# Optimization experiments

Measured on AMD Instinct MI355X. Metric: run time of the kernel, lower is better.

Reference implementation:

```python
import jax, jax.numpy as jnp
import numpy as np

BS, HS, NH = 8, 3, 8          # block_size, halo_size, num_heads
WIN = BS + 2 * HS             # 14
DQK = 16                      # dim_head_qk = make_divisible(128*1.0)//8
DV = 16                       # dim_head_v = 128 // 8
SCALE = DQK ** -0.5


def _rel_pos_index():
    # Faithful numpy port of QueryFreePosEmbedRel._get_relative_position_index
    w = WIN
    coords = np.stack(np.meshgrid(np.arange(w), np.arange(w), indexing='ij'))  # (2,w,w)
    flat = coords.reshape(2, -1)                                               # (2, w*w)
    rel = flat[:, :, None] - flat[:, None, :]                                  # (2, ww, ww)
    rel = rel.transpose(1, 2, 0).astype(np.int64)
    rel[:, :, 0] += w - 1
    rel[:, :, 1] += w - 1
    rel[:, :, 0] *= 2 * w - 1
    rel = rel.sum(-1).reshape(w, w, w, w)
    sh = (w - BS) // 2  # == halo_size
    rel = rel[sh:sh + BS, sh:sh + BS, :, :].reshape(BS * BS, w * w)
    return rel

_REL_IDX = _rel_pos_index()


def setup_inputs() -> dict:
    key = jax.random.key(0)
    k1, k2, k3, k4, k5, k6 = jax.random.split(key, 6)
    C = 128
    dim_out_qk = NH * DQK   # 128
    dim_out_v = NH * DV     # 128
    x = jax.random.normal(k1, (4, 128, 128, C), dtype=jnp.float32)
    q_w = jax.random.normal(k2, (dim_out_qk, C), dtype=jnp.float32) * 0.05
    kv_w = jax.random.normal(k3, (dim_out_qk + dim_out_v, C), dtype=jnp.float32) * 0.05
    pos_table = jax.random.normal(k4, ((2 * WIN - 1) * (2 * WIN - 1), NH), dtype=jnp.float32) * 0.02
    proj_w = jax.random.normal(k5, (dim_out_v, dim_out_v), dtype=jnp.float32) * 0.05
    proj_b = jax.random.normal(k6, (dim_out_v,), dtype=jnp.float32) * 0.01
    return {"x": x, "q_w": q_w, "kv_w": kv_w, "pos_table": pos_table,
            "proj_w": proj_w, "proj_b": proj_b}


def reference(x, q_w, kv_w, pos_table, proj_w, proj_b):
    B, H, W, C = x.shape  # H,W divisible by BS -> no padding branch
    nhb, nwb = H // BS, W // BS
    nb = nhb * nwb

    # --- queries: (B,NH,nb,bs^2,DQK), block-partitioned ---
    q = x @ q_w.T
    q = q.reshape(B, nhb, BS, nwb, BS, NH, DQK).transpose(0, 5, 1, 3, 2, 4, 6)
    q = q.reshape(B, NH, nb, BS * BS, DQK)

    # --- kv 1x1 conv + halo padding + overlapping window extraction ---
    kv = x @ kv_w.T                                   # (B,H,W, NH*(DQK+DV))
    kv = jnp.pad(kv, ((0, 0), (HS, HS), (HS, HS), (0, 0)))
    ri = (np.arange(nhb) * BS)[:, None] + np.arange(WIN)[None, :]
    ci = (np.arange(nwb) * BS)[:, None] + np.arange(WIN)[None, :]
    kvw = kv[:, ri]
    kvw = kvw[:, :, :, ci]
    kvw = kvw.transpose(0, 1, 3, 2, 4, 5).reshape(B, nb, WIN * WIN, NH, DQK + DV)
    kvw = kvw.transpose(0, 3, 1, 2, 4)
    k = kvw[..., :DQK]
    v = kvw[..., DQK:]

    bias = pos_table[_REL_IDX.reshape(-1)].reshape(BS * BS, WIN * WIN, NH)
    bias = bias.transpose(2, 0, 1)[None, :, None]

    # --- scores + halo-boundary mask + softmax ---
    attn = jnp.einsum('bhnqd,bhnkd->bhnqk', q * SCALE, k) + bias
    ones = jnp.pad(jnp.ones((H, W), jnp.float32), ((HS, HS), (HS, HS)))
    mw = ones[ri][:, :, ci].transpose(0, 2, 1, 3).reshape(nb, WIN * WIN)
    valid = (mw > 0)[None, None, :, None, :]
    attn = jnp.where(valid, attn, -jnp.finfo(attn.dtype).max)
    attn = jax.nn.softmax(attn, axis=-1)

    # --- weighted sum over V, fold blocks back to (B,H,W,dim_out_v) ---
    out = jnp.einsum('bhnqk,bhnkd->bhnqd', attn, v)   # (B,NH,nb,bs^2,DV)
    out = out.reshape(B, NH, nhb, nwb, BS, BS, DV)
    out = out.transpose(0, 2, 4, 3, 5, 1, 6).reshape(B, H, W, NH * DV)
    return out @ proj_w.T + proj_b
```

## Files before the change

kernel.cpp:

```cpp
#include <hip/hip_runtime.h>
#include <float.h>


typedef float f32x4 __attribute__((ext_vector_type(4)));
typedef short s16x4 __attribute__((ext_vector_type(4)));
typedef short s16x8 __attribute__((ext_vector_type(8)));
typedef unsigned int u32x2 __attribute__((ext_vector_type(2)));
typedef unsigned int u32x4 __attribute__((ext_vector_type(4)));

__device__ inline ushort f2bf(float f) {
    unsigned u = __float_as_uint(f);
    return (ushort)((u + 0x7FFF + ((u >> 16) & 1)) >> 16);
}
__device__ inline float bf2f(ushort h) { return __uint_as_float((unsigned)h << 16); }
__device__ inline unsigned cvtpk(float a, float b) {
    unsigned r;
    asm("v_cvt_pk_bf16_f32 %0, %1, %2" : "=v"(r) : "v"(a), "v"(b));
    return r;
}
#if __has_builtin(__builtin_amdgcn_exp2f)
#define EXP2(x) __builtin_amdgcn_exp2f(x)
#else
#define EXP2(x) exp2f(x)
#endif

__global__ __launch_bounds__(256) void conv_w(
    const float* __restrict__ q_w, const float* __restrict__ kv_w,
    const float* __restrict__ proj_w, ushort* whi, ushort* wlo)
{
    const int g = blockIdx.x * 256 + threadIdx.x;
    const int row = g >> 7, col = g & 127;
    const float v = (row < 128) ? q_w[row * 128 + col]
                  : (row < 384) ? kv_w[(row - 128) * 128 + col]
                                : proj_w[(row - 384) * 128 + col];
    const ushort h = f2bf(v);
    const int off = ((row >> 4) * 2048) + ((col >> 3) * 128) + ((row & 15) * 8) + (col & 7);
    whi[off] = h;
    wlo[off] = f2bf(v - bf2f(h));
}

__global__ __launch_bounds__(256) void gemm_split(
    const float* A,
    const ushort* __restrict__ Whi, const ushort* __restrict__ Wlo,
    int wbase, int ntc, int tok1,
    ushort* qb, ushort* kvb, float* outf, const float* __restrict__ bias)
{
    __shared__ ushort Ah[128 * 128];
    __shared__ ushort Al[128 * 128];

    const int t = threadIdx.x;
    const int row0 = blockIdx.x * 128;
    const int w = t >> 6, l = t & 63;
    const int wm = w >> 1, wn = w & 1;
    const int lr = l & 15, cA = l >> 4;

#pragma unroll
    for (int i = 0; i < 16; ++i) {
        const int idx = t + i * 256;
        const int p = idx >> 5, fc = idx & 31;
        const float4 v = *(const float4*)(A + (size_t)(row0 + p) * 128 + fc * 4);
        const int base = p * 128 + (((fc >> 1) ^ (p & 7)) << 3) + (fc & 1) * 4;
        const unsigned h01 = cvtpk(v.x, v.y), h23 = cvtpk(v.z, v.w);
        *(u32x2*)&Ah[base] = (u32x2){h01, h23};
        const float hx = __uint_as_float(h01 << 16);
        const float hy = __uint_as_float(h01 & 0xFFFF0000u);
        const float hz = __uint_as_float(h23 << 16);
        const float hw = __uint_as_float(h23 & 0xFFFF0000u);
        *(u32x2*)&Al[base] = (u32x2){ cvtpk(v.x - hx, v.y - hy),
                                      cvtpk(v.z - hz, v.w - hw) };
    }
    __syncthreads();

#pragma unroll 1
    for (int nt = 0; nt < ntc; ++nt) {
        f32x4 acc[4][4];
#pragma unroll
        for (int mf = 0; mf < 4; ++mf)
#pragma unroll
            for (int nf = 0; nf < 4; ++nf) acc[mf][nf] = (f32x4){0.f,0.f,0.f,0.f};

#pragma unroll 1
        for (int kk = 0; kk < 4; ++kk) {
            s16x8 wh[4], wl[4];
#pragma unroll
            for (int nf = 0; nf < 4; ++nf) {
                const int rb = (wbase >> 4) + nt * 8 + wn * 4 + nf;
                const size_t off = (size_t)rb * 2048 + (kk * 4 + cA) * 128 + lr * 8;
                wh[nf] = *(const s16x8*)&Whi[off];
                wl[nf] = *(const s16x8*)&Wlo[off];
            }
#pragma unroll
            for (int mf = 0; mf < 4; ++mf) {
                const int p = wm * 64 + mf * 16 + lr;
                const int off = p * 128 + ((((kk << 2) + cA) ^ (p & 7)) << 3);
                const s16x8 xh = *(const s16x8*)&Ah[off];
                const s16x8 xl = *(const s16x8*)&Al[off];
#pragma unroll
                for (int nf = 0; nf < 4; ++nf) {
                    acc[mf][nf] = __builtin_amdgcn_mfma_f32_16x16x32_bf16(
                                      wh[nf], xh, acc[mf][nf], 0, 0, 0);
                    acc[mf][nf] = __builtin_amdgcn_mfma_f32_16x16x32_bf16(
                                      wh[nf], xl, acc[mf][nf], 0, 0, 0);
                    acc[mf][nf] = __builtin_amdgcn_mfma_f32_16x16x32_bf16(
                                      wl[nf], xh, acc[mf][nf], 0, 0, 0);
                }
            }
        }

#pragma unroll
        for (int mf = 0; mf < 4; ++mf) {
            const size_t pix = row0 + wm * 64 + mf * 16 + lr;
#pragma unroll
            for (int nf = 0; nf < 4; ++nf) {
                const int chan = wn * 64 + nf * 16 + cA * 4;
                const f32x4 o = acc[mf][nf];
                if (tok1) {
                    const u32x2 pk = (u32x2){ cvtpk(o[0], o[1]), cvtpk(o[2], o[3]) };
                    if (nt == 0) {
                        const int head = wn * 4 + nf;
                        *(u32x2*)(qb + ((size_t)head << 20) + pix * 16 + (chan & 15)) = pk;
                    } else {
                        const int gchan = (nt - 1) * 128 + chan;
                        const int head = gchan >> 5;
                        *(u32x2*)(kvb + ((size_t)head << 21) + pix * 32 + (gchan & 31)) = pk;
                    }
                } else {
                    const float4 bv = *(const float4*)(bias + chan);
                    f32x4 r = o;
                    r[0] += bv.x; r[1] += bv.y; r[2] += bv.z; r[3] += bv.w;
                    *(f32x4*)(outf + pix * 128 + chan) = r;
                }
            }
        }
    }
}

__global__ __launch_bounds__(256) void halo_attn(
    float* out,
    const ushort* __restrict__ qg,
    const ushort* __restrict__ kvg,
    const float* __restrict__ pos_table)
{
    __shared__ ushort VT[2][16][232];
    __shared__ float  bias_l[444];
    __shared__ int    keyoff[256];
    __shared__ ushort vbf[232];

    const int t  = threadIdx.x;
    const int bi = blockIdx.x, head = blockIdx.y, bpair = blockIdx.z;
    const int by = bi >> 4, bx = bi & 15;
    const int w  = t >> 6;
    const int lb = w >> 1;
    const int qh = w & 1;
    const int batch = bpair * 2 + lb;
    const int l  = t & 63;
    const int lr = l & 15;
    const int cA = l >> 4;

    const char* kvh = (const char*)(kvg + ((size_t)head << 21) + ((size_t)batch << 19));

    if (t < 224) {
        const int wy = t >> 4, wx = t & 15;
        const int py = by * 8 + wy - 3, px = bx * 8 + wx - 3;
        const bool valid = (wx < 14) && ((unsigned)py < 128u) && ((unsigned)px < 128u);
        keyoff[t] = valid ? ((py * 128 + px) * 64) : 0;
        vbf[t]    = valid ? (ushort)0x3F80 : (ushort)0;
    } else {
        keyoff[t] = 0;
        if (t < 232) vbf[t] = 0;
    }
    for (int i = t; i < 444; i += 256) {
        float v = 0.f;
        if (i >= 2) {
            const int r = i - 2, ry = r / 21, rx = r - ry * 21;
            v = pos_table[((ry + 3) * 27 + rx + 3) * 8 + head] * 1.44269504f;
        }
        bias_l[i] = v;
    }
    __syncthreads();

#pragma unroll
    for (int it = 0; it < 2; ++it) {
        const int idx = t + it * 256;
        if (idx < 448) {
            const int slb = (idx < 224) ? 0 : 1;
            const int key = idx - slb * 224;
            const char* sb = (const char*)(kvg + ((size_t)head << 21)
                             + ((size_t)(bpair * 2 + slb) << 19));
            const char* src = sb + keyoff[key] + 32;
            const bool valid = vbf[key] != 0;
            const s16x8 z = (s16x8){0,0,0,0,0,0,0,0};
            const s16x8 v0 = valid ? *(const s16x8*)src : z;
            const s16x8 v1 = valid ? *(const s16x8*)(src + 16) : z;
#pragma unroll
            for (int j = 0; j < 8; ++j) {
                VT[slb][j][key]     = (ushort)v0[j];
                VT[slb][j + 8][key] = (ushort)v1[j];
            }
        }
    }
    __syncthreads();

    const int gbase = ((lr >> 2) << 3) + (lr & 3);
    const int wy0 = cA >> 1, wx0 = (cA & 1) * 8;
    const ushort* qhp = qg + ((size_t)head << 20);
    s16x8 qf[2];
    float* optr[2];
    const float* bptr[2];
#pragma unroll
    for (int j = 0; j < 2; ++j) {
        const int q = (qh * 2 + j) * 16 + lr;
        const int qy = q >> 3, qx = q & 7;
        const size_t pix = ((size_t)(batch * 128 + by * 8 + qy)) * 128 + bx * 8 + qx;
        optr[j] = out + pix * 128 + head * 16 + cA * 4;
        bptr[j] = bias_l + 2 + (qy + 13 - wy0) * 21 + (qx + 6 - wx0);
#pragma unroll
        for (int k = 0; k < 8; ++k) qf[j][k] = 0;
        if (cA < 2)
            qf[j] = *(const s16x8*)(qhp + pix * 16 + cA * 8);
    }

    f32x4 accv[2], accs[2];
#pragma unroll
    for (int j = 0; j < 2; ++j) {
        accv[j] = (f32x4){0.f, 0.f, 0.f, 0.f};
        accs[j] = (f32x4){0.f, 0.f, 0.f, 0.f};
    }

    s16x8 ak0 = *(const s16x8*)(kvh + keyoff[gbase]     + cA * 16);
    s16x8 ak1 = *(const s16x8*)(kvh + keyoff[gbase + 4] + cA * 16);

#pragma unroll 1
    for (int m = 0; m < 7; ++m) {
        const int nx = 32 * (m + 1) + gbase;
        const s16x8 nk0 = *(const s16x8*)(kvh + keyoff[nx]     + cA * 16);
        const s16x8 nk1 = *(const s16x8*)(kvh + keyoff[nx + 4] + cA * 16);

        const int kb = 32 * m + cA * 8;
        const s16x8 vt  = *(const s16x8*)&VT[lb][lr][kb];
        const s16x8 vld = *(const s16x8*)&vbf[kb];

#pragma unroll
        for (int j = 0; j < 2; ++j) {
            const f32x4 sf0 = __builtin_amdgcn_mfma_f32_16x16x32_bf16(
                                  ak0, qf[j], (f32x4){0.f, 0.f, 0.f, 0.f}, 0, 0, 0);
            const f32x4 sf1 = __builtin_amdgcn_mfma_f32_16x16x32_bf16(
                                  ak1, qf[j], (f32x4){0.f, 0.f, 0.f, 0.f}, 0, 0, 0);
            const float* bq = bptr[j] - m * 42;
            float pr0[4], pr1[4];
#pragma unroll
            for (int r = 0; r < 4; ++r)
                pr0[r] = EXP2(fmaf(sf0[r], 0.36067376f, bq[7 - r]));
#pragma unroll
            for (int r = 0; r < 4; ++r)
                pr1[r] = EXP2(fmaf(sf1[r], 0.36067376f, bq[3 - r]));

            const u32x4 pk = (u32x4){ cvtpk(pr0[0], pr0[1]), cvtpk(pr0[2], pr0[3]),
                                      cvtpk(pr1[0], pr1[1]), cvtpk(pr1[2], pr1[3]) };
            const s16x8 pb = *(const s16x8*)&pk;
            accv[j] = __builtin_amdgcn_mfma_f32_16x16x32_bf16(vt,  pb, accv[j], 0, 0, 0);
            accs[j] = __builtin_amdgcn_mfma_f32_16x16x32_bf16(vld, pb, accs[j], 0, 0, 0);
        }
        ak0 = nk0;
        ak1 = nk1;
    }

#pragma unroll
    for (int j = 0; j < 2; ++j) {
        const float inv = 1.0f / accs[j][0];
        *(f32x4*)optr[j] = accv[j] * inv;
    }
}

extern "C" void kernel_launch(void* const* d_in, const int* in_sizes, int n_in,
                              void* d_out, int out_size, void* d_ws, size_t ws_size,
                              hipStream_t stream) {
    const float* x      = (const float*)d_in[0];
    const float* q_w    = (const float*)d_in[1];
    const float* kv_w   = (const float*)d_in[2];
    const float* pt     = (const float*)d_in[3];
    const float* proj_w = (const float*)d_in[4];
    const float* proj_b = (const float*)d_in[5];
    float* out = (float*)d_out;

    ushort* ykvb = (ushort*)d_ws;
    ushort* qb   = (ushort*)((char*)d_ws + 33554432);
    ushort* whi  = (ushort*)((char*)d_ws + 33554432 + 16777216);
    ushort* wlo  = whi + 65536;

    const dim3 blk(256);
    conv_w<<<dim3(256), blk, 0, stream>>>(q_w, kv_w, proj_w, whi, wlo);
    gemm_split<<<dim3(512), blk, 0, stream>>>(x, whi, wlo, 0, 3, 1,
                                              qb, ykvb, nullptr, nullptr);
    halo_attn<<<dim3(256, 8, 2), blk, 0, stream>>>(out, qb, ykvb, pt);
    gemm_split<<<dim3(512), blk, 0, stream>>>(out, whi, wlo, 384, 1, 0,
                                              nullptr, nullptr, out, proj_b);
}
```

Before: 90.61 us.

## Process all four batches per halo_attn block and precompute bias table

The halo_attn kernel now uses 512-thread blocks that cover all four batch images for one spatial block and head, instead of two batches per block over a grid z of 2. The keyoff/vbf index setup and the bias table are therefore built once per block for more work. The exp2-scaled relative-position bias table is moved into the weight-conversion kernel, which writes it to workspace, and halo_attn only copies it into shared memory. In exchange there are half as many blocks, each with larger shared memory (VT doubles) and twice the threads, which may lower occupancy or scheduling flexibility.

```diff
diff --git a/kernel.cpp b/kernel.cpp
--- a/kernel.cpp
+++ b/kernel.cpp
@@ -26,17 +26,32 @@
 
 __global__ __launch_bounds__(256) void conv_w(
     const float* __restrict__ q_w, const float* __restrict__ kv_w,
-    const float* __restrict__ proj_w, ushort* whi, ushort* wlo)
+    const float* __restrict__ proj_w, const float* __restrict__ pos_table,
+    ushort* whi, ushort* wlo, float* bias_g)
 {
-    const int g = blockIdx.x * 256 + threadIdx.x;
-    const int row = g >> 7, col = g & 127;
-    const float v = (row < 128) ? q_w[row * 128 + col]
-                  : (row < 384) ? kv_w[(row - 128) * 128 + col]
-                                : proj_w[(row - 384) * 128 + col];
-    const ushort h = f2bf(v);
-    const int off = ((row >> 4) * 2048) + ((col >> 3) * 128) + ((row & 15) * 8) + (col & 7);
-    whi[off] = h;
-    wlo[off] = f2bf(v - bf2f(h));
+    if (blockIdx.x < 256) {
+        const int g = blockIdx.x * 256 + threadIdx.x;
+        const int row = g >> 7, col = g & 127;
+        const float v = (row < 128) ? q_w[row * 128 + col]
+                      : (row < 384) ? kv_w[(row - 128) * 128 + col]
+                                    : proj_w[(row - 384) * 128 + col];
+        const ushort h = f2bf(v);
+        const int off = ((row >> 4) * 2048) + ((col >> 3) * 128)
+                      + ((row & 15) * 8) + (col & 7);
+        whi[off] = h;
+        wlo[off] = f2bf(v - bf2f(h));
+    } else {
+        const int i = (blockIdx.x - 256) * 256 + threadIdx.x;
+        if (i < 8 * 448) {
+            const int h = i / 448, e = i - h * 448;
+            float v = 0.f;
+            if (e >= 2) {
+                const int r = e - 2, ry = r / 21, rx = r - ry * 21;
+                v = pos_table[((ry + 3) * 27 + rx + 3) * 8 + h] * 1.44269504f;
+            }
+            bias_g[h * 448 + e] = v;
+        }
+    }
 }
 
 __global__ __launch_bounds__(256) void gemm_split(
@@ -135,29 +150,28 @@
     }
 }
 
-__global__ __launch_bounds__(256) void halo_attn(
+__global__ __launch_bounds__(512) void halo_attn(
     float* out,
     const ushort* __restrict__ qg,
     const ushort* __restrict__ kvg,
-    const float* __restrict__ pos_table)
+    const float* __restrict__ bias_g)
 {
-    __shared__ ushort VT[2][16][232];
-    __shared__ float  bias_l[444];
+    __shared__ ushort VT[4][16][232];
+    __shared__ float  bias_l[448];
     __shared__ int    keyoff[256];
     __shared__ ushort vbf[232];
 
     const int t  = threadIdx.x;
-    const int bi = blockIdx.x, head = blockIdx.y, bpair = blockIdx.z;
+    const int bi = blockIdx.x, head = blockIdx.y;
     const int by = bi >> 4, bx = bi & 15;
     const int w  = t >> 6;
     const int lb = w >> 1;
     const int qh = w & 1;
-    const int batch = bpair * 2 + lb;
     const int l  = t & 63;
     const int lr = l & 15;
     const int cA = l >> 4;
 
-    const char* kvh = (const char*)(kvg + ((size_t)head << 21) + ((size_t)batch << 19));
+    const char* kvh = (const char*)(kvg + ((size_t)head << 21) + ((size_t)lb << 19));
 
     if (t < 224) {
         const int wy = t >> 4, wx = t & 15;
@@ -165,28 +179,21 @@
         const bool valid = (wx < 14) && ((unsigned)py < 128u) && ((unsigned)px < 128u);
         keyoff[t] = valid ? ((py * 128 + px) * 64) : 0;
         vbf[t]    = valid ? (ushort)0x3F80 : (ushort)0;
-    } else {
+    } else if (t < 256) {
         keyoff[t] = 0;
         if (t < 232) vbf[t] = 0;
     }
-    for (int i = t; i < 444; i += 256) {
-        float v = 0.f;
-        if (i >= 2) {
-            const int r = i - 2, ry = r / 21, rx = r - ry * 21;
-            v = pos_table[((ry + 3) * 27 + rx + 3) * 8 + head] * 1.44269504f;
-        }
-        bias_l[i] = v;
-    }
+    for (int i = t; i < 448; i += 512)
+        bias_l[i] = bias_g[head * 448 + i];
     __syncthreads();
 
 #pragma unroll
-    for (int it = 0; it < 2; ++it) {
-        const int idx = t + it * 256;
-        if (idx < 448) {
-            const int slb = (idx < 224) ? 0 : 1;
-            const int key = idx - slb * 224;
+    for (int rd = 0; rd < 2; ++rd) {
+        const int key = (t & 127) + rd * 128;
+        const int slb = t >> 7;
+        if (key < 224) {
             const char* sb = (const char*)(kvg + ((size_t)head << 21)
-                             + ((size_t)(bpair * 2 + slb) << 19));
+                             + ((size_t)slb << 19));
             const char* src = sb + keyoff[key] + 32;
             const bool valid = vbf[key] != 0;
             const s16x8 z = (s16x8){0,0,0,0,0,0,0,0};
@@ -211,7 +218,7 @@
     for (int j = 0; j < 2; ++j) {
         const int q = (qh * 2 + j) * 16 + lr;
         const int qy = q >> 3, qx = q & 7;
-        const size_t pix = ((size_t)(batch * 128 + by * 8 + qy)) * 128 + bx * 8 + qx;
+        const size_t pix = ((size_t)(lb * 128 + by * 8 + qy)) * 128 + bx * 8 + qx;
         optr[j] = out + pix * 128 + head * 16 + cA * 4;
         bptr[j] = bias_l + 2 + (qy + 13 - wy0) * 21 + (qx + 6 - wx0);
 #pragma unroll
@@ -287,12 +294,13 @@
     ushort* qb   = (ushort*)((char*)d_ws + 33554432);
     ushort* whi  = (ushort*)((char*)d_ws + 33554432 + 16777216);
     ushort* wlo  = whi + 65536;
-
-    const dim3 blk(256);
-    conv_w<<<dim3(256), blk, 0, stream>>>(q_w, kv_w, proj_w, whi, wlo);
-    gemm_split<<<dim3(512), blk, 0, stream>>>(x, whi, wlo, 0, 3, 1,
-                                              qb, ykvb, nullptr, nullptr);
-    halo_attn<<<dim3(256, 8, 2), blk, 0, stream>>>(out, qb, ykvb, pt);
-    gemm_split<<<dim3(512), blk, 0, stream>>>(out, whi, wlo, 384, 1, 0,
-                                              nullptr, nullptr, out, proj_b);
-}
+    float*  bias_g = (float*)(wlo + 65536);
+
+    conv_w<<<dim3(270), dim3(256), 0, stream>>>(q_w, kv_w, proj_w, pt,
+                                                whi, wlo, bias_g);
+    gemm_split<<<dim3(512), dim3(256), 0, stream>>>(x, whi, wlo, 0, 3, 1,
+                                                    qb, ykvb, nullptr, nullptr);
+    halo_attn<<<dim3(256, 8), dim3(512), 0, stream>>>(out, qb, ykvb, bias_g);
+    gemm_split<<<dim3(512), dim3(256), 0, stream>>>(out, whi, wlo, 384, 1, 0,
+                                                    nullptr, nullptr, out, proj_b);
+}
```

Result: faster. 87.86 us (median of 2 runs) (-3.0%).
